# Optimization experiments

Measured on AMD Instinct MI355X. Metric: run time of the kernel, lower is better.

The kernel has to match this reference:

```python
import jax, jax.numpy as jnp
import numpy as np

EPS = 1e-5
TEMP = 0.07
LARGE_NEG = -1e9


def mi_net(x, W1, g1, b1, W2, b2, Ws, lng, lnb):
    # x: (B, C, T). 1x1 convs == per-position channel projections.
    y = jnp.einsum('bct,oc->bot', x, W1)                      # conv1 (no bias)
    mu = y.mean(axis=(0, 2), keepdims=True)                   # BatchNorm2d, training-mode batch stats
    var = y.var(axis=(0, 2), keepdims=True)
    y = (y - mu) * jax.lax.rsqrt(var + EPS) * g1[None, :, None] + b1[None, :, None]
    y = jax.nn.relu(y)
    y = jnp.einsum('bot,po->bpt', y, W2) + b2[None, :, None]  # conv2 (bias)
    h = y + jnp.einsum('bct,oc->bot', x, Ws)                  # linear shortcut
    mu2 = h.mean(axis=1, keepdims=True)                       # LayerNorm over channel dim
    v2 = h.var(axis=1, keepdims=True)
    return (h - mu2) * jax.lax.rsqrt(v2 + EPS) * lng[None, :, None] + lnb[None, :, None]


def infonce(L, G):
    # L: (N, D, T) locals, G: (N, D) single global per sample (n_multis = 1)
    N, D, T = L.shape
    l_p = jnp.swapaxes(L, 1, 2)                               # (N, T, D)
    l_p = l_p / jnp.linalg.norm(l_p, axis=2, keepdims=True)
    g = G / jnp.linalg.norm(G, axis=1, keepdims=True)         # (N, D)
    u_p = (jnp.einsum('ntd,nd->nt', l_p, g) / TEMP)[:, :, None]   # (N, T, 1), positives scaled by temp
    # negatives: <global_i, local_{j,t}>; NOT divided by temperature (faithful to torch source)
    u_n = jnp.einsum('nd,mtd->nmt', g, l_p)                   # (N, N, T)
    eye = jnp.eye(N, dtype=bool)[:, :, None]
    u_n = jnp.where(eye, LARGE_NEG, u_n).reshape(N, N * T)    # mask self pairs
    logits = jnp.concatenate(
        [u_p, jnp.broadcast_to(u_n[:, None, :], (N, T, N * T))], axis=2)  # (N, T, 1+N*T)
    logp = jax.nn.log_softmax(logits, axis=2)
    return -logp[:, :, 0].mean()


def setup_inputs() -> dict:
    key = jax.random.key(0)
    ks = jax.random.split(key, 10)
    B, CL, CG, T, MI = 32, 1536, 192, 256, 512
    d = {
        'local_feat': jax.random.normal(ks[0], (B, CL, T), jnp.float32),
        'global_feat': jax.random.normal(ks[1], (B, CG), jnp.float32),
        # local_net params
        'lW1': jax.random.normal(ks[2], (MI, CL), jnp.float32) * 0.02,
        'lg1': jnp.ones((MI,), jnp.float32),
        'lb1': jnp.zeros((MI,), jnp.float32),
        'lW2': jax.random.normal(ks[3], (MI, MI), jnp.float32) * 0.02,
        'lb2': jnp.zeros((MI,), jnp.float32),
        'lWs': jax.random.normal(ks[4], (MI, CL), jnp.float32) * 0.02,
        'llng': jnp.ones((MI,), jnp.float32),
        'llnb': jnp.zeros((MI,), jnp.float32),
        # global_net params (global_channels != mi_units -> net exists)
        'gW1': jax.random.normal(ks[5], (MI, CG), jnp.float32) * 0.02,
        'gg1': jnp.ones((MI,), jnp.float32),
        'gb1': jnp.zeros((MI,), jnp.float32),
        'gW2': jax.random.normal(ks[6], (MI, MI), jnp.float32) * 0.02,
        'gb2': jnp.zeros((MI,), jnp.float32),
    }
    # shortcut with near-identity init (n_units >= n_input for global net)
    gWs = jax.random.uniform(ks[7], (MI, CG), jnp.float32, -0.01, 0.01)
    gWs = gWs.at[jnp.arange(CG), jnp.arange(CG)].set(1.0)
    d['gWs'] = gWs
    d['glng'] = jnp.ones((MI,), jnp.float32)
    d['glnb'] = jnp.zeros((MI,), jnp.float32)
    return d


def reference(local_feat, global_feat,
              lW1, lg1, lb1, lW2, lb2, lWs, llng, llnb,
              gW1, gg1, gb1, gW2, gb2, gWs, glng, glnb):
    L = mi_net(local_feat, lW1, lg1, lb1, lW2, lb2, lWs, llng, llnb)      # (B, MI, T)
    G = mi_net(global_feat[:, :, None], gW1, gg1, gb1, gW2, gb2, gWs, glng, glnb)[:, :, 0]  # (B, MI)
    return infonce(L, G)
```

## Files before the change

kernel.cpp:

```cpp
#include <hip/hip_runtime.h>

#define B 32
#define CL 1536
#define CG 192
#define T 256
#define MI 512
#define NPOS 8192
#define EPS 1e-5f
#define TEMP 0.07f

typedef __attribute__((ext_vector_type(8))) __bf16 bf16x8;
typedef __attribute__((ext_vector_type(4))) float f32x4;

__device__ __forceinline__ unsigned short f2bf(float f) {
  union { float f; unsigned u; } v; v.f = f;
  unsigned r = v.u + 0x7FFFu + ((v.u >> 16) & 1u);
  return (unsigned short)(r >> 16);
}
__device__ __forceinline__ float bf2f(unsigned short h) {
  union { unsigned u; float f; } v; v.u = ((unsigned)h) << 16;
  return v.f;
}

__device__ __forceinline__ float wave_sum(float v) {
#pragma unroll
  for (int off = 32; off > 0; off >>= 1) v += __shfl_xor(v, off, 64);
  return v;
}
__device__ __forceinline__ float block_sum(float v, float* rb) {
  v = wave_sum(v);
  __syncthreads();
  if ((threadIdx.x & 63) == 0) rb[threadIdx.x >> 6] = v;
  __syncthreads();
  return rb[0] + rb[1] + rb[2] + rb[3];
}
__device__ __forceinline__ float bs128(float v, float* rb) {
  v = wave_sum(v);
  __syncthreads();
  if ((threadIdx.x & 63) == 0) rb[threadIdx.x >> 6] = v;
  __syncthreads();
  return rb[0] + rb[1];
}

__global__ __launch_bounds__(256) void k_prep(
    const float* __restrict__ x, const float* __restrict__ lW1,
    const float* __restrict__ lWs, const float* __restrict__ lW2,
    const float* __restrict__ gx, const float* __restrict__ gW1,
    unsigned short* __restrict__ xT, unsigned short* __restrict__ Wc,
    unsigned short* __restrict__ W2b, float* __restrict__ y1g,
    float* __restrict__ bsum) {
  __shared__ float xs[64][65];
  const int bi = blockIdx.x, tid = threadIdx.x;
  if (bi < 1792) {
    int idx = (bi * 256 + tid) * 4;
    const float* src; unsigned short* dst;
    if (idx < 786432) { src = lW1 + idx; dst = Wc + idx; }
    else if (idx < 1572864) { src = lWs + (idx - 786432); dst = Wc + idx; }
    else { src = lW2 + (idx - 1572864); dst = W2b + (idx - 1572864); }
    float4 v = *(const float4*)src;
    ushort4 o = {f2bf(v.x), f2bf(v.y), f2bf(v.z), f2bf(v.w)};
    *(ushort4*)dst = o;
  } else if (bi < 4864) {
    int bi2 = bi - 1792;
    int b = bi2 / 96, rem = bi2 - b * 96;
    int c0 = (rem >> 2) * 64, t0 = (rem & 3) * 64;
    const float* xb = x + ((size_t)b * CL + c0) * T + t0;
#pragma unroll
    for (int i = 0; i < 16; i++) {
      int idx = tid + i * 256, c = idx >> 6, t = idx & 63;
      xs[c][t] = xb[(size_t)c * T + t];
    }
    __syncthreads();
    unsigned short* ob = xT + ((size_t)b * T + t0) * CL + c0;
#pragma unroll
    for (int i = 0; i < 8; i++) {
      int idx = tid + i * 256, t = idx >> 5, k = (idx & 31) * 2;
      ushort2 v = {f2bf(xs[k][t]), f2bf(xs[k + 1][t])};
      *(ushort2*)&ob[(size_t)t * CL + k] = v;
    }
  } else if (bi < 4928) {
    int idx = (bi - 4864) * 256 + tid;
    int b = idx & 31, o = idx >> 5;
    float s = 0.f;
    for (int c = 0; c < CG; c++) s = fmaf(gx[b * CG + c], gW1[o * CG + c], s);
    y1g[o * 32 + b] = s;
  } else {
    float4 z = {0.f, 0.f, 0.f, 0.f};
    ((float4*)bsum)[tid] = z;
  }
}

__global__ __launch_bounds__(128, 4) void k_gemm1(
    const unsigned short* __restrict__ xT, const unsigned short* __restrict__ Wc,
    unsigned short* __restrict__ y1u, unsigned short* __restrict__ ysb,
    float* __restrict__ bsum, float* __restrict__ bsq,
    const float* __restrict__ y1g, const float* __restrict__ gg1,
    const float* __restrict__ gb1, const float* __restrict__ gW2,
    const float* __restrict__ gb2, const float* __restrict__ gx,
    const float* __restrict__ gWsc, float* __restrict__ hg) {
  const int tid = threadIdx.x, bi = blockIdx.x;
  if (bi >= 2048) {
    __shared__ float gsc[512], gsh[512];
#pragma unroll
    for (int jj = 0; jj < 4; jj++) {
      int o = tid + jj * 128;
      float s = 0.f, s2 = 0.f;
      for (int b = 0; b < 32; b++) {
        float v = y1g[o * 32 + b];
        s += v; s2 = fmaf(v, v, s2);
      }
      float mu = s * (1.f / 32.f);
      float var = s2 * (1.f / 32.f) - mu * mu;
      float sc = gg1[o] * rsqrtf(var + EPS);
      gsc[o] = sc;
      gsh[o] = gb1[o] - mu * sc;
    }
    __syncthreads();
    int base = (bi - 2048) * 256;
#pragma unroll
    for (int jj = 0; jj < 2; jj++) {
      int idx = base + jj * 128 + tid;
      int b = idx & 31, p = idx >> 5;
      float s = gb2[p];
      for (int o = 0; o < MI; o++) {
        float v = fmaxf(fmaf(y1g[o * 32 + b], gsc[o], gsh[o]), 0.f);
        s = fmaf(v, gW2[(size_t)p * MI + o], s);
      }
      for (int c = 0; c < CG; c++) s = fmaf(gx[b * CG + c], gWsc[p * CG + c], s);
      hg[p * 32 + b] = s;
    }
    return;
  }
  __shared__ __align__(16) unsigned short As[64][32];
  __shared__ __align__(16) unsigned short Bs[64][32];
  __shared__ float ps[64], pq[64];
  const int w = tid >> 6, lane = tid & 63;
  const int m0 = (bi & 127) * 64, o0 = (bi >> 7) * 64;
  const int sr = lane >> 2, sc = (lane & 3) * 8;
  const int lm = lane & 15, q = lane >> 4;
  f32x4 acc[4][2];
#pragma unroll
  for (int i = 0; i < 4; i++)
#pragma unroll
    for (int j = 0; j < 2; j++) acc[i][j] = f32x4{0.f, 0.f, 0.f, 0.f};

  const unsigned short* pa = xT + (size_t)(m0 + w * 32 + sr) * CL + sc;
  const unsigned short* pb = Wc + (size_t)(o0 + w * 32 + sr) * CL + sc;
  for (int k0 = 0; k0 < CL; k0 += 32) {
    __builtin_amdgcn_global_load_lds(
        (const __attribute__((address_space(1))) void*)(pa + k0),
        (__attribute__((address_space(3))) void*)&As[w * 32][0], 16, 0, 0);
    __builtin_amdgcn_global_load_lds(
        (const __attribute__((address_space(1))) void*)(pa + 16 * CL + k0),
        (__attribute__((address_space(3))) void*)&As[w * 32 + 16][0], 16, 0, 0);
    __builtin_amdgcn_global_load_lds(
        (const __attribute__((address_space(1))) void*)(pb + k0),
        (__attribute__((address_space(3))) void*)&Bs[w * 32][0], 16, 0, 0);
    __builtin_amdgcn_global_load_lds(
        (const __attribute__((address_space(1))) void*)(pb + 16 * CL + k0),
        (__attribute__((address_space(3))) void*)&Bs[w * 32 + 16][0], 16, 0, 0);
    __syncthreads();
    bf16x8 af[4], bfr[2];
#pragma unroll
    for (int mi = 0; mi < 4; mi++)
      af[mi] = *(const bf16x8*)&As[mi * 16 + lm][q * 8];
#pragma unroll
    for (int ni = 0; ni < 2; ni++)
      bfr[ni] = *(const bf16x8*)&Bs[w * 32 + ni * 16 + lm][q * 8];
#pragma unroll
    for (int mi = 0; mi < 4; mi++)
#pragma unroll
      for (int ni = 0; ni < 2; ni++)
        acc[mi][ni] = __builtin_amdgcn_mfma_f32_16x16x32_bf16(
            af[mi], bfr[ni], acc[mi][ni], 0, 0, 0);
    __syncthreads();
  }
  const int row0 = m0 + q * 4;
  const bool isY1 = (o0 < 512);
  unsigned short* dst = isY1 ? y1u : ysb;
  const int ob = isY1 ? o0 : o0 - 512;
#pragma unroll
  for (int mi = 0; mi < 4; mi++)
#pragma unroll
    for (int ni = 0; ni < 2; ni++) {
      int oc = ob + w * 32 + ni * 16 + lm;
#pragma unroll
      for (int r = 0; r < 4; r++)
        dst[(size_t)(row0 + mi * 16 + r) * 512 + oc] = f2bf(acc[mi][ni][r]);
    }
  if (isY1) {
#pragma unroll
    for (int ni = 0; ni < 2; ni++) {
      float s = 0.f, s2 = 0.f;
#pragma unroll
      for (int mi = 0; mi < 4; mi++)
#pragma unroll
        for (int r = 0; r < 4; r++) {
          float v = acc[mi][ni][r];
          s += v; s2 = fmaf(v, v, s2);
        }
      s += __shfl_xor(s, 16, 64);  s2 += __shfl_xor(s2, 16, 64);
      s += __shfl_xor(s, 32, 64);  s2 += __shfl_xor(s2, 32, 64);
      if (q == 0) {
        int c = w * 32 + ni * 16 + lm;
        ps[c] = s; pq[c] = s2;
      }
    }
    __syncthreads();
    if (tid < 64) {
      atomicAdd(&bsum[o0 + tid], ps[tid]);
      atomicAdd(&bsq[o0 + tid], pq[tid]);
    }
  }
}

__global__ __launch_bounds__(256) void k_bnapp(
    const unsigned short* __restrict__ y1u, const float* __restrict__ bsum,
    const float* __restrict__ bsq, const float* __restrict__ lg1,
    const float* __restrict__ lb1, unsigned short* __restrict__ vv) {
  int idx = (blockIdx.x * 256 + threadIdx.x) * 4;
  int o = idx & 511;
  ushort4 in = *(const ushort4*)&y1u[idx];
  float iv[4] = {bf2f(in.x), bf2f(in.y), bf2f(in.z), bf2f(in.w)};
  unsigned short ov[4];
#pragma unroll
  for (int j = 0; j < 4; j++) {
    float mu = bsum[o + j] * (1.f / NPOS);
    float var = bsq[o + j] * (1.f / NPOS) - mu * mu;
    float sc = lg1[o + j] * rsqrtf(var + EPS);
    float sh = lb1[o + j] - mu * sc;
    ov[j] = f2bf(fmaxf(fmaf(iv[j], sc, sh), 0.f));
  }
  ushort4 out = {ov[0], ov[1], ov[2], ov[3]};
  *(ushort4*)&vv[idx] = out;
}

__global__ __launch_bounds__(128, 4) void k_gemm2(
    const unsigned short* __restrict__ vv, const unsigned short* __restrict__ W2b,
    const float* __restrict__ b2, const unsigned short* __restrict__ ysb,
    unsigned short* __restrict__ hb16,
    const float* __restrict__ hg, const float* __restrict__ glng,
    const float* __restrict__ glnb, unsigned short* __restrict__ gnormb) {
  __shared__ __align__(16) unsigned short As[64][32];
  __shared__ __align__(16) unsigned short Bs[64][32];
  __shared__ float rb[2];
  const int tid = threadIdx.x, bi = blockIdx.x;
  if (bi >= 1024) {
    int b = bi - 1024;
    float v[4], Lv[4];
    float s = 0.f, s2 = 0.f;
#pragma unroll
    for (int j = 0; j < 4; j++) {
      v[j] = hg[(tid + j * 128) * 32 + b];
      s += v[j]; s2 = fmaf(v[j], v[j], s2);
    }
    s = bs128(s, rb);
    s2 = bs128(s2, rb);
    float mu = s * (1.f / MI);
    float var = s2 * (1.f / MI) - mu * mu;
    float rstd = rsqrtf(var + EPS);
    float n2 = 0.f;
#pragma unroll
    for (int j = 0; j < 4; j++) {
      int p = tid + j * 128;
      Lv[j] = fmaf((v[j] - mu) * rstd, glng[p], glnb[p]);
      n2 = fmaf(Lv[j], Lv[j], n2);
    }
    n2 = bs128(n2, rb);
    float inv = rsqrtf(n2);
#pragma unroll
    for (int j = 0; j < 4; j++)
      gnormb[b * MI + tid + j * 128] = f2bf(Lv[j] * inv);
    return;
  }
  const int w = tid >> 6, lane = tid & 63;
  const int m0 = (bi & 127) * 64, p0 = (bi >> 7) * 64;
  const int sr = lane >> 2, sc = (lane & 3) * 8;
  const int lm = lane & 15, q = lane >> 4;
  f32x4 acc[4][2];
#pragma unroll
  for (int i = 0; i < 4; i++)
#pragma unroll
    for (int j = 0; j < 2; j++) acc[i][j] = f32x4{0.f, 0.f, 0.f, 0.f};

  const unsigned short* pa = vv + (size_t)(m0 + w * 32 + sr) * 512 + sc;
  const unsigned short* pb = W2b + (size_t)(p0 + w * 32 + sr) * 512 + sc;
  for (int k0 = 0; k0 < 512; k0 += 32) {
    __builtin_amdgcn_global_load_lds(
        (const __attribute__((address_space(1))) void*)(pa + k0),
        (__attribute__((address_space(3))) void*)&As[w * 32][0], 16, 0, 0);
    __builtin_amdgcn_global_load_lds(
        (const __attribute__((address_space(1))) void*)(pa + 16 * 512 + k0),
        (__attribute__((address_space(3))) void*)&As[w * 32 + 16][0], 16, 0, 0);
    __builtin_amdgcn_global_load_lds(
        (const __attribute__((address_space(1))) void*)(pb + k0),
        (__attribute__((address_space(3))) void*)&Bs[w * 32][0], 16, 0, 0);
    __builtin_amdgcn_global_load_lds(
        (const __attribute__((address_space(1))) void*)(pb + 16 * 512 + k0),
        (__attribute__((address_space(3))) void*)&Bs[w * 32 + 16][0], 16, 0, 0);
    __syncthreads();
    bf16x8 af[4], bfr[2];
#pragma unroll
    for (int mi = 0; mi < 4; mi++)
      af[mi] = *(const bf16x8*)&As[mi * 16 + lm][q * 8];
#pragma unroll
    for (int ni = 0; ni < 2; ni++)
      bfr[ni] = *(const bf16x8*)&Bs[w * 32 + ni * 16 + lm][q * 8];
#pragma unroll
    for (int mi = 0; mi < 4; mi++)
#pragma unroll
      for (int ni = 0; ni < 2; ni++)
        acc[mi][ni] = __builtin_amdgcn_mfma_f32_16x16x32_bf16(
            af[mi], bfr[ni], acc[mi][ni], 0, 0, 0);
    __syncthreads();
  }
  const int row0 = m0 + q * 4;
#pragma unroll
  for (int ni = 0; ni < 2; ni++) {
    int p = p0 + w * 32 + ni * 16 + lm;
    float bias = b2[p];
#pragma unroll
    for (int mi = 0; mi < 4; mi++)
#pragma unroll
      for (int r = 0; r < 4; r++) {
        size_t off = (size_t)(row0 + mi * 16 + r) * 512 + p;
        hb16[off] = f2bf(acc[mi][ni][r] + bias + bf2f(ysb[off]));
      }
  }
}

__global__ __launch_bounds__(256) void k_tail(
    const unsigned short* __restrict__ hb16, const float* __restrict__ lng,
    const float* __restrict__ lnb, const unsigned short* __restrict__ gnormb,
    float* __restrict__ up, float* __restrict__ pmax, float* __restrict__ psum) {
  __shared__ __align__(16) unsigned short gs[32 * 512];
  __shared__ __align__(16) unsigned short Ls[32 * 512];
  __shared__ float Ured[4 * 1024];
  const int tid = threadIdx.x;
  const int w = tid >> 6, lane = tid & 63;
  const int r0 = blockIdx.x * 32;
  const int smp = r0 >> 8;
#pragma unroll
  for (int i = 0; i < 8; i++) {
    int e = (tid + i * 256) * 8;
    *(uint4*)&gs[e] = *(const uint4*)&gnormb[e];
  }
  float4 g0 = *(const float4*)&lng[lane * 8];
  float4 g1 = *(const float4*)&lng[lane * 8 + 4];
  float4 bb0 = *(const float4*)&lnb[lane * 8];
  float4 bb1 = *(const float4*)&lnb[lane * 8 + 4];
  float gg[8] = {g0.x, g0.y, g0.z, g0.w, g1.x, g1.y, g1.z, g1.w};
  float bz[8] = {bb0.x, bb0.y, bb0.z, bb0.w, bb1.x, bb1.y, bb1.z, bb1.w};
#pragma unroll
  for (int j = 0; j < 8; j++) {
    int rr = w * 8 + j;
    const unsigned short* row = hb16 + (size_t)(r0 + rr) * 512 + lane * 8;
    ushort4 u0 = *(const ushort4*)row;
    ushort4 u1 = *(const ushort4*)(row + 4);
    float v[8] = {bf2f(u0.x), bf2f(u0.y), bf2f(u0.z), bf2f(u0.w),
                  bf2f(u1.x), bf2f(u1.y), bf2f(u1.z), bf2f(u1.w)};
    float s = 0.f, s2 = 0.f;
#pragma unroll
    for (int k = 0; k < 8; k++) { s += v[k]; s2 = fmaf(v[k], v[k], s2); }
    s = wave_sum(s);
    s2 = wave_sum(s2);
    float mu = s * (1.f / MI);
    float var = s2 * (1.f / MI) - mu * mu;
    float rstd = rsqrtf(var + EPS);
    float L[8], n2 = 0.f;
#pragma unroll
    for (int k = 0; k < 8; k++) {
      L[k] = fmaf((v[k] - mu) * rstd, gg[k], bz[k]);
      n2 = fmaf(L[k], L[k], n2);
    }
    n2 = wave_sum(n2);
    float inv = rsqrtf(n2);
    unsigned short* orow = &Ls[rr * 512 + lane * 8];
    ushort4 o0 = {f2bf(L[0] * inv), f2bf(L[1] * inv), f2bf(L[2] * inv), f2bf(L[3] * inv)};
    ushort4 o1 = {f2bf(L[4] * inv), f2bf(L[5] * inv), f2bf(L[6] * inv), f2bf(L[7] * inv)};
    *(ushort4*)orow = o0;
    *(ushort4*)(orow + 4) = o1;
  }
  __syncthreads();
  const int lm = lane & 15, q = lane >> 4;
  f32x4 acc[2][2];
#pragma unroll
  for (int i = 0; i < 2; i++)
#pragma unroll
    for (int j = 0; j < 2; j++) acc[i][j] = f32x4{0.f, 0.f, 0.f, 0.f};
#pragma unroll
  for (int kk = 0; kk < 4; kk++) {
    int k0 = w * 128 + kk * 32 + q * 8;
    bf16x8 af[2], bfr[2];
#pragma unroll
    for (int mi = 0; mi < 2; mi++)
      af[mi] = *(const bf16x8*)&gs[(mi * 16 + lm) * 512 + k0];
#pragma unroll
    for (int ni = 0; ni < 2; ni++)
      bfr[ni] = *(const bf16x8*)&Ls[(ni * 16 + lm) * 512 + k0];
#pragma unroll
    for (int mi = 0; mi < 2; mi++)
#pragma unroll
      for (int ni = 0; ni < 2; ni++)
        acc[mi][ni] = __builtin_amdgcn_mfma_f32_16x16x32_bf16(
            af[mi], bfr[ni], acc[mi][ni], 0, 0, 0);
  }
#pragma unroll
  for (int mi = 0; mi < 2; mi++)
#pragma unroll
    for (int ni = 0; ni < 2; ni++)
#pragma unroll
      for (int r = 0; r < 4; r++) {
        int m = mi * 16 + q * 4 + r, n = ni * 16 + lm;
        Ured[w * 1024 + m * 32 + n] = acc[mi][ni][r];
      }
  __syncthreads();
  float u[4];
#pragma unroll
  for (int j = 0; j < 4; j++) {
    int idx = tid * 4 + j;
    u[j] = Ured[idx] + Ured[1024 + idx] + Ured[2048 + idx] + Ured[3072 + idx];
  }
  __syncthreads();
#pragma unroll
  for (int j = 0; j < 4; j++) Ured[tid * 4 + j] = u[j];
  int m = (tid * 4) >> 5;
  if (m == smp) {
#pragma unroll
    for (int j = 0; j < 4; j++)
      up[r0 + ((tid * 4 + j) & 31)] = u[j] * (1.f / TEMP);
  }
  __syncthreads();
  if (tid < 32) {
    float mx = -1e30f, s = 0.f;
    if (tid != smp) {
      for (int n = 0; n < 32; n++) mx = fmaxf(mx, Ured[tid * 32 + n]);
      for (int n = 0; n < 32; n++) s += expf(Ured[tid * 32 + n] - mx);
    }
    pmax[tid * 256 + blockIdx.x] = mx;
    psum[tid * 256 + blockIdx.x] = s;
  }
}

__global__ __launch_bounds__(256) void k_loss(
    const float* __restrict__ up, const float* __restrict__ pmax,
    const float* __restrict__ psum, float* __restrict__ out) {
  __shared__ float rb[4];
  __shared__ float red[32][8];
  __shared__ float Ms[32], Ss[32];
  const int tid = threadIdx.x;
  const int n = tid >> 3, j = tid & 7;
  float mx = -1e30f;
  for (int c = j * 32; c < j * 32 + 32; c++) mx = fmaxf(mx, pmax[n * 256 + c]);
  red[n][j] = mx;
  __syncthreads();
  if (j == 0) {
    float M = -1e30f;
#pragma unroll
    for (int k = 0; k < 8; k++) M = fmaxf(M, red[n][k]);
    Ms[n] = M;
  }
  __syncthreads();
  float M = Ms[n];
  float s = 0.f;
  for (int c = j * 32; c < j * 32 + 32; c++)
    s += psum[n * 256 + c] * expf(pmax[n * 256 + c] - M);
  __syncthreads();
  red[n][j] = s;
  __syncthreads();
  if (j == 0) {
    float S = 0.f;
#pragma unroll
    for (int k = 0; k < 8; k++) S += red[n][k];
    Ss[n] = S;
  }
  __syncthreads();
  float acc = 0.f;
  for (int i = tid; i < NPOS; i += 256) {
    int nn = i >> 8;
    float upv = up[i];
    float Mn = Ms[nn], Sn = Ss[nn];
    float mx2 = fmaxf(upv, Mn);
    float lse = mx2 + logf(expf(upv - mx2) + Sn * expf(Mn - mx2));
    acc += lse - upv;
  }
  acc = block_sum(acc, rb);
  if (tid == 0) out[0] = acc * (1.f / NPOS);
}

extern "C" void kernel_launch(void* const* d_in, const int* in_sizes, int n_in,
                              void* d_out, int out_size, void* d_ws, size_t ws_size,
                              hipStream_t stream) {
  (void)in_sizes; (void)n_in; (void)out_size; (void)ws_size;
  const float* x    = (const float*)d_in[0];
  const float* gx   = (const float*)d_in[1];
  const float* lW1  = (const float*)d_in[2];
  const float* lg1  = (const float*)d_in[3];
  const float* lb1  = (const float*)d_in[4];
  const float* lW2  = (const float*)d_in[5];
  const float* lb2  = (const float*)d_in[6];
  const float* lWs  = (const float*)d_in[7];
  const float* llng = (const float*)d_in[8];
  const float* llnb = (const float*)d_in[9];
  const float* gW1  = (const float*)d_in[10];
  const float* gg1  = (const float*)d_in[11];
  const float* gb1  = (const float*)d_in[12];
  const float* gW2  = (const float*)d_in[13];
  const float* gb2  = (const float*)d_in[14];
  const float* gWs  = (const float*)d_in[15];
  const float* glng = (const float*)d_in[16];
  const float* glnb = (const float*)d_in[17];

  char* wsb = (char*)d_ws;
  unsigned short* xT     = (unsigned short*)(wsb);
  unsigned short* Wc     = (unsigned short*)(wsb + 25165824);
  unsigned short* W2b    = (unsigned short*)(wsb + 28311552);
  unsigned short* y1u    = (unsigned short*)(wsb + 28835840);
  unsigned short* ysb    = (unsigned short*)(wsb + 37224448);
  unsigned short* vv     = (unsigned short*)(wsb + 45613056);
  unsigned short* hb16   = (unsigned short*)(wsb + 54001664);
  float* bsum            = (float*)(wsb + 71827456);
  float* bsq             = (float*)(wsb + 71829504);
  float* y1g             = (float*)(wsb + 71831552);
  float* hg              = (float*)(wsb + 71901184);
  unsigned short* gnormb = (unsigned short*)(wsb + 71966720);
  float* up              = (float*)(wsb + 71999488);
  float* pmax            = (float*)(wsb + 72032256);
  float* psum            = (float*)(wsb + 72065024);

  k_prep<<<dim3(4929), 256, 0, stream>>>(x, lW1, lWs, lW2, gx, gW1, xT, Wc, W2b,
                                         y1g, bsum);
  k_gemm1<<<dim3(2112), 128, 0, stream>>>(xT, Wc, y1u, ysb, bsum, bsq,
                                          y1g, gg1, gb1, gW2, gb2, gx, gWs, hg);
  k_bnapp<<<dim3(4096), 256, 0, stream>>>(y1u, bsum, bsq, lg1, lb1, vv);
  k_gemm2<<<dim3(1056), 128, 0, stream>>>(vv, W2b, lb2, ysb, hb16,
                                          hg, glng, glnb, gnormb);
  k_tail<<<dim3(256), 256, 0, stream>>>(hb16, llng, llnb, gnormb, up, pmax, psum);
  k_loss<<<dim3(1), 256, 0, stream>>>(up, pmax, psum, (float*)d_out);
}
```

Measured before the change: 254.2 us.

## Fuse BN-apply into GEMM2, enlarge GEMM tiles with swizzled LDS, vectorize transpose

Removes the separate k_bnapp kernel: GEMM2 now computes the BatchNorm scale/shift per channel and applies BN+ReLU while staging A tiles into LDS. Both GEMMs move to 64x128 tiles with K-step 64 and an XOR-swizzled LDS layout, which raises MFMA work per load and is meant to avoid bank conflicts. The shortcut add moves from the GEMM2 epilogue into k_tail. The xT transpose writes 16-byte vectors instead of 4-byte pairs. In exchange, register use rises and occupancy is lowered to 2 blocks per SM.

```diff
diff --git a/kernel.cpp b/kernel.cpp
--- a/kernel.cpp
+++ b/kernel.cpp
@@ -73,10 +73,17 @@
     __syncthreads();
     unsigned short* ob = xT + ((size_t)b * T + t0) * CL + c0;
 #pragma unroll
-    for (int i = 0; i < 8; i++) {
-      int idx = tid + i * 256, t = idx >> 5, k = (idx & 31) * 2;
-      ushort2 v = {f2bf(xs[k][t]), f2bf(xs[k + 1][t])};
-      *(ushort2*)&ob[(size_t)t * CL + k] = v;
+    for (int half = 0; half < 2; half++) {
+      int s = tid + half * 256;
+      int t = s >> 3, kg = s & 7;
+      unsigned short v[8];
+#pragma unroll
+      for (int j = 0; j < 8; j++) v[j] = f2bf(xs[kg * 8 + j][t]);
+      uint4 o = {(unsigned)v[0] | ((unsigned)v[1] << 16),
+                 (unsigned)v[2] | ((unsigned)v[3] << 16),
+                 (unsigned)v[4] | ((unsigned)v[5] << 16),
+                 (unsigned)v[6] | ((unsigned)v[7] << 16)};
+      *(uint4*)&ob[(size_t)t * CL + kg * 8] = o;
     }
   } else if (bi < 4928) {
     int idx = (bi - 4864) * 256 + tid;
@@ -90,7 +97,7 @@
   }
 }
 
-__global__ __launch_bounds__(128, 4) void k_gemm1(
+__global__ __launch_bounds__(128, 2) void k_gemm1(
     const unsigned short* __restrict__ xT, const unsigned short* __restrict__ Wc,
     unsigned short* __restrict__ y1u, unsigned short* __restrict__ ysb,
     float* __restrict__ bsum, float* __restrict__ bsq,
@@ -99,7 +106,7 @@
     const float* __restrict__ gb2, const float* __restrict__ gx,
     const float* __restrict__ gWsc, float* __restrict__ hg) {
   const int tid = threadIdx.x, bi = blockIdx.x;
-  if (bi >= 2048) {
+  if (bi >= 1024) {
     __shared__ float gsc[512], gsh[512];
 #pragma unroll
     for (int jj = 0; jj < 4; jj++) {
@@ -116,7 +123,7 @@
       gsh[o] = gb1[o] - mu * sc;
     }
     __syncthreads();
-    int base = (bi - 2048) * 256;
+    int base = (bi - 1024) * 256;
 #pragma unroll
     for (int jj = 0; jj < 2; jj++) {
       int idx = base + jj * 128 + tid;
@@ -131,48 +138,52 @@
     }
     return;
   }
-  __shared__ __align__(16) unsigned short As[64][32];
-  __shared__ __align__(16) unsigned short Bs[64][32];
-  __shared__ float ps[64], pq[64];
+  __shared__ __align__(16) unsigned short As[64 * 64];
+  __shared__ __align__(16) unsigned short Bs[128 * 64];
+  __shared__ float ps[128], pq[128];
   const int w = tid >> 6, lane = tid & 63;
-  const int m0 = (bi & 127) * 64, o0 = (bi >> 7) * 64;
-  const int sr = lane >> 2, sc = (lane & 3) * 8;
+  const int m0 = (bi & 127) * 64, o0 = (bi >> 7) * 128;
+  const int r8 = lane >> 3;
+  const int csw = ((lane & 7) ^ r8) * 8;
   const int lm = lane & 15, q = lane >> 4;
-  f32x4 acc[4][2];
+  const int sw0 = lm & 7;
+  f32x4 acc[4][4];
 #pragma unroll
   for (int i = 0; i < 4; i++)
 #pragma unroll
-    for (int j = 0; j < 2; j++) acc[i][j] = f32x4{0.f, 0.f, 0.f, 0.f};
-
-  const unsigned short* pa = xT + (size_t)(m0 + w * 32 + sr) * CL + sc;
-  const unsigned short* pb = Wc + (size_t)(o0 + w * 32 + sr) * CL + sc;
-  for (int k0 = 0; k0 < CL; k0 += 32) {
-    __builtin_amdgcn_global_load_lds(
-        (const __attribute__((address_space(1))) void*)(pa + k0),
-        (__attribute__((address_space(3))) void*)&As[w * 32][0], 16, 0, 0);
-    __builtin_amdgcn_global_load_lds(
-        (const __attribute__((address_space(1))) void*)(pa + 16 * CL + k0),
-        (__attribute__((address_space(3))) void*)&As[w * 32 + 16][0], 16, 0, 0);
-    __builtin_amdgcn_global_load_lds(
-        (const __attribute__((address_space(1))) void*)(pb + k0),
-        (__attribute__((address_space(3))) void*)&Bs[w * 32][0], 16, 0, 0);
-    __builtin_amdgcn_global_load_lds(
-        (const __attribute__((address_space(1))) void*)(pb + 16 * CL + k0),
-        (__attribute__((address_space(3))) void*)&Bs[w * 32 + 16][0], 16, 0, 0);
-    __syncthreads();
-    bf16x8 af[4], bfr[2];
-#pragma unroll
-    for (int mi = 0; mi < 4; mi++)
-      af[mi] = *(const bf16x8*)&As[mi * 16 + lm][q * 8];
-#pragma unroll
-    for (int ni = 0; ni < 2; ni++)
-      bfr[ni] = *(const bf16x8*)&Bs[w * 32 + ni * 16 + lm][q * 8];
-#pragma unroll
-    for (int mi = 0; mi < 4; mi++)
-#pragma unroll
-      for (int ni = 0; ni < 2; ni++)
-        acc[mi][ni] = __builtin_amdgcn_mfma_f32_16x16x32_bf16(
-            af[mi], bfr[ni], acc[mi][ni], 0, 0, 0);
+    for (int j = 0; j < 4; j++) acc[i][j] = f32x4{0.f, 0.f, 0.f, 0.f};
+
+  const unsigned short* pa = xT + (size_t)(m0 + w * 32 + r8) * CL + csw;
+  const unsigned short* pb = Wc + (size_t)(o0 + w * 64 + r8) * CL + csw;
+  for (int k0 = 0; k0 < CL; k0 += 64) {
+#pragma unroll
+    for (int i = 0; i < 4; i++)
+      __builtin_amdgcn_global_load_lds(
+          (const __attribute__((address_space(1))) void*)(pa + (size_t)i * 8 * CL + k0),
+          (__attribute__((address_space(3))) void*)&As[(w * 32 + i * 8) * 64], 16, 0, 0);
+#pragma unroll
+    for (int i = 0; i < 8; i++)
+      __builtin_amdgcn_global_load_lds(
+          (const __attribute__((address_space(1))) void*)(pb + (size_t)i * 8 * CL + k0),
+          (__attribute__((address_space(3))) void*)&Bs[(w * 64 + i * 8) * 64], 16, 0, 0);
+    __syncthreads();
+#pragma unroll
+    for (int kc = 0; kc < 2; kc++) {
+      const int ch = ((kc * 4 + q) ^ sw0) * 8;
+      bf16x8 af[4], bfr[4];
+#pragma unroll
+      for (int mi = 0; mi < 4; mi++)
+        af[mi] = *(const bf16x8*)&As[(mi * 16 + lm) * 64 + ch];
+#pragma unroll
+      for (int ni = 0; ni < 4; ni++)
+        bfr[ni] = *(const bf16x8*)&Bs[(w * 64 + ni * 16 + lm) * 64 + ch];
+#pragma unroll
+      for (int mi = 0; mi < 4; mi++)
+#pragma unroll
+        for (int ni = 0; ni < 4; ni++)
+          acc[mi][ni] = __builtin_amdgcn_mfma_f32_16x16x32_bf16(
+              af[mi], bfr[ni], acc[mi][ni], 0, 0, 0);
+    }
     __syncthreads();
   }
   const int row0 = m0 + q * 4;
@@ -182,15 +193,15 @@
 #pragma unroll
   for (int mi = 0; mi < 4; mi++)
 #pragma unroll
-    for (int ni = 0; ni < 2; ni++) {
-      int oc = ob + w * 32 + ni * 16 + lm;
+    for (int ni = 0; ni < 4; ni++) {
+      int oc = ob + w * 64 + ni * 16 + lm;
 #pragma unroll
       for (int r = 0; r < 4; r++)
         dst[(size_t)(row0 + mi * 16 + r) * 512 + oc] = f2bf(acc[mi][ni][r]);
     }
   if (isY1) {
 #pragma unroll
-    for (int ni = 0; ni < 2; ni++) {
+    for (int ni = 0; ni < 4; ni++) {
       float s = 0.f, s2 = 0.f;
 #pragma unroll
       for (int mi = 0; mi < 4; mi++)
@@ -202,51 +213,30 @@
       s += __shfl_xor(s, 16, 64);  s2 += __shfl_xor(s2, 16, 64);
       s += __shfl_xor(s, 32, 64);  s2 += __shfl_xor(s2, 32, 64);
       if (q == 0) {
-        int c = w * 32 + ni * 16 + lm;
+        int c = w * 64 + ni * 16 + lm;
         ps[c] = s; pq[c] = s2;
       }
     }
     __syncthreads();
-    if (tid < 64) {
-      atomicAdd(&bsum[o0 + tid], ps[tid]);
-      atomicAdd(&bsq[o0 + tid], pq[tid]);
-    }
-  }
-}
-
-__global__ __launch_bounds__(256) void k_bnapp(
-    const unsigned short* __restrict__ y1u, const float* __restrict__ bsum,
-    const float* __restrict__ bsq, const float* __restrict__ lg1,
-    const float* __restrict__ lb1, unsigned short* __restrict__ vv) {
-  int idx = (blockIdx.x * 256 + threadIdx.x) * 4;
-  int o = idx & 511;
-  ushort4 in = *(const ushort4*)&y1u[idx];
-  float iv[4] = {bf2f(in.x), bf2f(in.y), bf2f(in.z), bf2f(in.w)};
-  unsigned short ov[4];
-#pragma unroll
-  for (int j = 0; j < 4; j++) {
-    float mu = bsum[o + j] * (1.f / NPOS);
-    float var = bsq[o + j] * (1.f / NPOS) - mu * mu;
-    float sc = lg1[o + j] * rsqrtf(var + EPS);
-    float sh = lb1[o + j] - mu * sc;
-    ov[j] = f2bf(fmaxf(fmaf(iv[j], sc, sh), 0.f));
-  }
-  ushort4 out = {ov[0], ov[1], ov[2], ov[3]};
-  *(ushort4*)&vv[idx] = out;
-}
-
-__global__ __launch_bounds__(128, 4) void k_gemm2(
-    const unsigned short* __restrict__ vv, const unsigned short* __restrict__ W2b,
-    const float* __restrict__ b2, const unsigned short* __restrict__ ysb,
-    unsigned short* __restrict__ hb16,
+    atomicAdd(&bsum[o0 + tid], ps[tid]);
+    atomicAdd(&bsq[o0 + tid], pq[tid]);
+  }
+}
+
+__global__ __launch_bounds__(128, 2) void k_gemm2(
+    const unsigned short* __restrict__ y1u, const unsigned short* __restrict__ W2b,
+    const float* __restrict__ bsum, const float* __restrict__ bsq,
+    const float* __restrict__ lg1, const float* __restrict__ lb1,
+    const float* __restrict__ b2, unsigned short* __restrict__ hb16,
     const float* __restrict__ hg, const float* __restrict__ glng,
     const float* __restrict__ glnb, unsigned short* __restrict__ gnormb) {
-  __shared__ __align__(16) unsigned short As[64][32];
-  __shared__ __align__(16) unsigned short Bs[64][32];
+  __shared__ __align__(16) unsigned short As[64 * 64];
+  __shared__ __align__(16) unsigned short Bs[128 * 64];
+  __shared__ float scl[512], shf[512];
   __shared__ float rb[2];
   const int tid = threadIdx.x, bi = blockIdx.x;
-  if (bi >= 1024) {
-    int b = bi - 1024;
+  if (bi >= 512) {
+    int b = bi - 512;
     float v[4], Lv[4];
     float s = 0.f, s2 = 0.f;
 #pragma unroll
@@ -274,64 +264,99 @@
     return;
   }
   const int w = tid >> 6, lane = tid & 63;
-  const int m0 = (bi & 127) * 64, p0 = (bi >> 7) * 64;
-  const int sr = lane >> 2, sc = (lane & 3) * 8;
+  const int m0 = (bi & 127) * 64, p0 = (bi >> 7) * 128;
+  const int r8 = lane >> 3;
+  const int csw = ((lane & 7) ^ r8) * 8;
   const int lm = lane & 15, q = lane >> 4;
-  f32x4 acc[4][2];
+  const int sw0 = lm & 7;
+#pragma unroll
+  for (int jj = 0; jj < 4; jj++) {
+    int ch = tid + jj * 128;
+    float mu = bsum[ch] * (1.f / NPOS);
+    float var = bsq[ch] * (1.f / NPOS) - mu * mu;
+    float sc = lg1[ch] * rsqrtf(var + EPS);
+    scl[ch] = sc;
+    shf[ch] = lb1[ch] - mu * sc;
+  }
+  __syncthreads();
+  f32x4 acc[4][4];
 #pragma unroll
   for (int i = 0; i < 4; i++)
 #pragma unroll
-    for (int j = 0; j < 2; j++) acc[i][j] = f32x4{0.f, 0.f, 0.f, 0.f};
-
-  const unsigned short* pa = vv + (size_t)(m0 + w * 32 + sr) * 512 + sc;
-  const unsigned short* pb = W2b + (size_t)(p0 + w * 32 + sr) * 512 + sc;
-  for (int k0 = 0; k0 < 512; k0 += 32) {
-    __builtin_amdgcn_global_load_lds(
-        (const __attribute__((address_space(1))) void*)(pa + k0),
-        (__attribute__((address_space(3))) void*)&As[w * 32][0], 16, 0, 0);
-    __builtin_amdgcn_global_load_lds(
-        (const __attribute__((address_space(1))) void*)(pa + 16 * 512 + k0),
-        (__attribute__((address_space(3))) void*)&As[w * 32 + 16][0], 16, 0, 0);
-    __builtin_amdgcn_global_load_lds(
-        (const __attribute__((address_space(1))) void*)(pb + k0),
-        (__attribute__((address_space(3))) void*)&Bs[w * 32][0], 16, 0, 0);
-    __builtin_amdgcn_global_load_lds(
-        (const __attribute__((address_space(1))) void*)(pb + 16 * 512 + k0),
-        (__attribute__((address_space(3))) void*)&Bs[w * 32 + 16][0], 16, 0, 0);
-    __syncthreads();
-    bf16x8 af[4], bfr[2];
-#pragma unroll
-    for (int mi = 0; mi < 4; mi++)
-      af[mi] = *(const bf16x8*)&As[mi * 16 + lm][q * 8];
-#pragma unroll
-    for (int ni = 0; ni < 2; ni++)
-      bfr[ni] = *(const bf16x8*)&Bs[w * 32 + ni * 16 + lm][q * 8];
-#pragma unroll
-    for (int mi = 0; mi < 4; mi++)
-#pragma unroll
-      for (int ni = 0; ni < 2; ni++)
-        acc[mi][ni] = __builtin_amdgcn_mfma_f32_16x16x32_bf16(
-            af[mi], bfr[ni], acc[mi][ni], 0, 0, 0);
+    for (int j = 0; j < 4; j++) acc[i][j] = f32x4{0.f, 0.f, 0.f, 0.f};
+
+  const int cg = tid & 7, rbase = tid >> 3;
+  const unsigned short* pb = W2b + (size_t)(p0 + w * 64 + r8) * 512 + csw;
+  for (int k0 = 0; k0 < 512; k0 += 64) {
+#pragma unroll
+    for (int i = 0; i < 8; i++)
+      __builtin_amdgcn_global_load_lds(
+          (const __attribute__((address_space(1))) void*)(pb + (size_t)i * 8 * 512 + k0),
+          (__attribute__((address_space(3))) void*)&Bs[(w * 64 + i * 8) * 64], 16, 0, 0);
+    float sreg[8], hreg[8];
+#pragma unroll
+    for (int j = 0; j < 8; j++) {
+      sreg[j] = scl[k0 + cg * 8 + j];
+      hreg[j] = shf[k0 + cg * 8 + j];
+    }
+#pragma unroll
+    for (int pass = 0; pass < 4; pass++) {
+      int row = rbase + pass * 16;
+      uint4 u = *(const uint4*)&y1u[(size_t)(m0 + row) * 512 + k0 + cg * 8];
+      unsigned short iv[8] = {
+          (unsigned short)(u.x & 0xffff), (unsigned short)(u.x >> 16),
+          (unsigned short)(u.y & 0xffff), (unsigned short)(u.y >> 16),
+          (unsigned short)(u.z & 0xffff), (unsigned short)(u.z >> 16),
+          (unsigned short)(u.w & 0xffff), (unsigned short)(u.w >> 16)};
+      unsigned short ov[8];
+#pragma unroll
+      for (int j = 0; j < 8; j++)
+        ov[j] = f2bf(fmaxf(fmaf(bf2f(iv[j]), sreg[j], hreg[j]), 0.f));
+      uint4 o = {(unsigned)ov[0] | ((unsigned)ov[1] << 16),
+                 (unsigned)ov[2] | ((unsigned)ov[3] << 16),
+                 (unsigned)ov[4] | ((unsigned)ov[5] << 16),
+                 (unsigned)ov[6] | ((unsigned)ov[7] << 16)};
+      *(uint4*)&As[row * 64 + ((cg ^ (row & 7)) * 8)] = o;
+    }
+    __syncthreads();
+#pragma unroll
+    for (int kc = 0; kc < 2; kc++) {
+      const int ch = ((kc * 4 + q) ^ sw0) * 8;
+      bf16x8 af[4], bfr[4];
+#pragma unroll
+      for (int mi = 0; mi < 4; mi++)
+        af[mi] = *(const bf16x8*)&As[(mi * 16 + lm) * 64 + ch];
+#pragma unroll
+      for (int ni = 0; ni < 4; ni++)
+        bfr[ni] = *(const bf16x8*)&Bs[(w * 64 + ni * 16 + lm) * 64 + ch];
+#pragma unroll
+      for (int mi = 0; mi < 4; mi++)
+#pragma unroll
+        for (int ni = 0; ni < 4; ni++)
+          acc[mi][ni] = __builtin_amdgcn_mfma_f32_16x16x32_bf16(
+              af[mi], bfr[ni], acc[mi][ni], 0, 0, 0);
+    }
     __syncthreads();
   }
   const int row0 = m0 + q * 4;
 #pragma unroll
-  for (int ni = 0; ni < 2; ni++) {
-    int p = p0 + w * 32 + ni * 16 + lm;
+  for (int ni = 0; ni < 4; ni++) {
+    int p = p0 + w * 64 + ni * 16 + lm;
     float bias = b2[p];
 #pragma unroll
     for (int mi = 0; mi < 4; mi++)
 #pragma unroll
       for (int r = 0; r < 4; r++) {
         size_t off = (size_t)(row0 + mi * 16 + r) * 512 + p;
-        hb16[off] = f2bf(acc[mi][ni][r] + bias + bf2f(ysb[off]));
+        hb16[off] = f2bf(acc[mi][ni][r] + bias);
       }
   }
 }
 
 __global__ __launch_bounds__(256) void k_tail(
-    const unsigned short* __restrict__ hb16, const float* __restrict__ lng,
-    const float* __restrict__ lnb, const unsigned short* __restrict__ gnormb,
+    const unsigned short* __restrict__ hb16, const unsigned short* __restrict__ ysb,
+    const float* __restrict__ lng, const float* __restrict__ lnb,
+    const unsigned short* __restrict__ gnormb,
     float* __restrict__ up, float* __restrict__ pmax, float* __restrict__ psum) {
   __shared__ __align__(16) unsigned short gs[32 * 512];
   __shared__ __align__(16) unsigned short Ls[32 * 512];
@@ -354,14 +379,26 @@
 #pragma unroll
   for (int j = 0; j < 8; j++) {
     int rr = w * 8 + j;
-    const unsigned short* row = hb16 + (size_t)(r0 + rr) * 512 + lane * 8;
-    ushort4 u0 = *(const ushort4*)row;
-    ushort4 u1 = *(const ushort4*)(row + 4);
-    float v[8] = {bf2f(u0.x), bf2f(u0.y), bf2f(u0.z), bf2f(u0.w),
-                  bf2f(u1.x), bf2f(u1.y), bf2f(u1.z), bf2f(u1.w)};
+    size_t off = (size_t)(r0 + rr) * 512 + lane * 8;
+    uint4 hu = *(const uint4*)&hb16[off];
+    uint4 yu = *(const uint4*)&ysb[off];
+    unsigned short hv[8] = {
+        (unsigned short)(hu.x & 0xffff), (unsigned short)(hu.x >> 16),
+        (unsigned short)(hu.y & 0xffff), (unsigned short)(hu.y >> 16),
+        (unsigned short)(hu.z & 0xffff), (unsigned short)(hu.z >> 16),
+        (unsigned short)(hu.w & 0xffff), (unsigned short)(hu.w >> 16)};
+    unsigned short yv[8] = {
+        (unsigned short)(yu.x & 0xffff), (unsigned short)(yu.x >> 16),
+        (unsigned short)(yu.y & 0xffff), (unsigned short)(yu.y >> 16),
+        (unsigned short)(yu.z & 0xffff), (unsigned short)(yu.z >> 16),
+        (unsigned short)(yu.w & 0xffff), (unsigned short)(yu.w >> 16)};
+    float v[8];
     float s = 0.f, s2 = 0.f;
 #pragma unroll
-    for (int k = 0; k < 8; k++) { s += v[k]; s2 = fmaf(v[k], v[k], s2); }
+    for (int k = 0; k < 8; k++) {
+      v[k] = bf2f(hv[k]) + bf2f(yv[k]);
+      s += v[k]; s2 = fmaf(v[k], v[k], s2);
+    }
     s = wave_sum(s);
     s2 = wave_sum(s2);
     float mu = s * (1.f / MI);
@@ -517,7 +554,6 @@
   unsigned short* W2b    = (unsigned short*)(wsb + 28311552);
   unsigned short* y1u    = (unsigned short*)(wsb + 28835840);
   unsigned short* ysb    = (unsigned short*)(wsb + 37224448);
-  unsigned short* vv     = (unsigned short*)(wsb + 45613056);
   unsigned short* hb16   = (unsigned short*)(wsb + 54001664);
   float* bsum            = (float*)(wsb + 71827456);
   float* bsq             = (float*)(wsb + 71829504);
@@ -530,11 +566,11 @@
 
   k_prep<<<dim3(4929), 256, 0, stream>>>(x, lW1, lWs, lW2, gx, gW1, xT, Wc, W2b,
                                          y1g, bsum);
-  k_gemm1<<<dim3(2112), 128, 0, stream>>>(xT, Wc, y1u, ysb, bsum, bsq,
+  k_gemm1<<<dim3(1088), 128, 0, stream>>>(xT, Wc, y1u, ysb, bsum, bsq,
                                           y1g, gg1, gb1, gW2, gb2, gx, gWs, hg);
-  k_bnapp<<<dim3(4096), 256, 0, stream>>>(y1u, bsum, bsq, lg1, lb1, vv);
-  k_gemm2<<<dim3(1056), 128, 0, stream>>>(vv, W2b, lb2, ysb, hb16,
-                                          hg, glng, glnb, gnormb);
-  k_tail<<<dim3(256), 256, 0, stream>>>(hb16, llng, llnb, gnormb, up, pmax, psum);
+  k_gemm2<<<dim3(544), 128, 0, stream>>>(y1u, W2b, bsum, bsq, lg1, lb1, lb2,
+                                         hb16, hg, glng, glnb, gnormb);
+  k_tail<<<dim3(256), 256, 0, stream>>>(hb16, ysb, llng, llnb, gnormb,
+                                        up, pmax, psum);
   k_loss<<<dim3(1), 256, 0, stream>>>(up, pmax, psum, (float*)d_out);
 }
```

Result: faster. 233.7 us (-8.0%).
